# Kernel optimization log

Hardware: AMD Instinct MI355X
Metric: run time of the kernel (lower is better)

## Reference

```python
import jax, jax.numpy as jnp
import numpy as np
import math

DIM_IN = 2
DIM_HIDDEN = 64
DIM_OUT = 16
NUM_LAYERS = 5  # num_layers-1 = 4 hidden SirenLayers per subnet + 1 last layer
W0 = 30.0
W0_INITIAL = 30.0
S0 = 0.0
C = 6.0
N_POINTS = 262144


def wire(w0, s0, z):
    # sin(w0*z) * exp(-(s0*z)^2)
    return jnp.sin(w0 * z) * jnp.exp(-jnp.square(s0 * z))


def setup_inputs() -> dict:
    key = jax.random.key(0)
    ks = jax.random.split(key, 8)
    # NOTE: source passes is_first=False for every layer, so init bound is
    # sqrt(c/dim_in)/layer_w0 for ALL layers (including the first).
    std0 = math.sqrt(C / DIM_IN) / W0_INITIAL
    stdh = math.sqrt(C / DIM_HIDDEN) / W0
    stdl = math.sqrt(C / DIM_HIDDEN) / W0
    u = lambda k, shape, s: jax.random.uniform(k, shape, jnp.float32, -s, s)
    nmid = NUM_LAYERS - 2  # hidden->hidden layers per subnet (3)
    return {
        "x": jax.random.uniform(ks[0], (N_POINTS, DIM_IN), jnp.float32),
        "W0m": u(ks[1], (DIM_OUT, DIM_HIDDEN, DIM_IN), std0),
        "b0": u(ks[2], (DIM_OUT, DIM_HIDDEN), std0),
        "Wm": u(ks[3], (nmid, DIM_OUT, DIM_HIDDEN, DIM_HIDDEN), stdh),
        "bm": u(ks[4], (nmid, DIM_OUT, DIM_HIDDEN), stdh),
        "Wl": u(ks[5], (DIM_OUT, DIM_HIDDEN), stdl),
        "bl": u(ks[6], (DIM_OUT,), stdl),
    }


def reference(x, W0m, b0, Wm, bm, Wl, bl):
    # First layer of each subnet (uses w0_initial): [N,D] x [O,H,D] -> [N,O,H]
    h = wire(W0_INITIAL, S0, jnp.einsum("nd,ohd->noh", x, W0m) + b0)
    # Middle hidden layers (w0), scanned over the fixed layer stack.
    def body(h, wb):
        W, b = wb
        h = wire(W0, S0, jnp.einsum("noh,ogh->nog", h, W) + b)
        return h, None
    h, _ = jax.lax.scan(body, h, (Wm, bm))
    # Last layer per subnet: dim 1 output each, is_last -> +0.5, no activation.
    out = jnp.einsum("noh,oh->no", h, Wl) + bl + 0.5  # [N, dim_out]
    return out
```

## Files before the change

### kernel.cpp

```cpp
#include <hip/hip_runtime.h>

typedef short bf16x8 __attribute__((ext_vector_type(8)));
typedef float f32x16 __attribute__((ext_vector_type(16)));
typedef float f32x2  __attribute__((ext_vector_type(2)));

#define NBGROUPS 128
#define SCALE 4.7746482927568601f

union Frag { bf16x8 v; unsigned u[4]; uint4 q; };

__device__ __forceinline__ unsigned pk_bf16(float lo, float hi) {
    unsigned r;
    asm("v_cvt_pk_bf16_f32 %0, %1, %2" : "=v"(r) : "v"(lo), "v"(hi));
    return r;
}
__device__ __forceinline__ float lo_f(unsigned w) { return __uint_as_float(w << 16); }
__device__ __forceinline__ float hi_f(unsigned w) { return __uint_as_float(w & 0xffff0000u); }

__device__ __forceinline__ f32x2 sin2(f32x2 z) {
    f32x2 r  = { rintf(z.x), rintf(z.y) };
    f32x2 v  = z - r;
    f32x2 v2 = v * v;
    f32x2 p  = { 32.765379f, 32.765379f };
    p = __builtin_elementwise_fma(p, v2, (f32x2){-74.468884f, -74.468884f});
    p = __builtin_elementwise_fma(p, v2, (f32x2){ 81.365064f,  81.365064f});
    p = __builtin_elementwise_fma(p, v2, (f32x2){-41.331084f, -41.331084f});
    p = __builtin_elementwise_fma(p, v2, (f32x2){  6.2830526f,  6.2830526f});
    return p * v;
}

struct BiasRegs { f32x2 p[2][8]; };
__device__ __forceinline__ BiasRegs load_bias(const float4* ldsBias, int Lb, int hi) {
    BiasRegs br;
#pragma unroll
    for (int tg = 0; tg < 2; ++tg) {
        const float4* base = &ldsBias[((Lb*2+tg)*2 + hi)*4];
#pragma unroll
        for (int q = 0; q < 4; ++q) {
            float4 b = base[q];
            br.p[tg][2*q]   = (f32x2){b.x, b.y};
            br.p[tg][2*q+1] = (f32x2){b.z, b.w};
        }
    }
    return br;
}

__device__ __forceinline__ void transitionHL(const f32x16* acc, const BiasRegs& br,
                                             Frag* Bhi, Frag* Blo) {
#pragma unroll
    for (int tg = 0; tg < 2; ++tg)
#pragma unroll
        for (int j = 0; j < 8; ++j) {
            f32x2 z = (f32x2){ acc[tg][2*j], acc[tg][2*j+1] } + br.p[tg][j];
            f32x2 s = sin2(z);
            unsigned ph = pk_bf16(s.x, s.y);
            f32x2 hf = { lo_f(ph), hi_f(ph) };
            f32x2 d  = s - hf;
            Bhi[tg*2 + (j>>2)].u[j&3] = ph;
            Blo[tg*2 + (j>>2)].u[j&3] = pk_bf16(d.x, d.y);
        }
}
__device__ __forceinline__ void transitionH(const f32x16* acc, const BiasRegs& br, Frag* Bhi) {
#pragma unroll
    for (int tg = 0; tg < 2; ++tg)
#pragma unroll
        for (int j = 0; j < 8; ++j) {
            f32x2 z = (f32x2){ acc[tg][2*j], acc[tg][2*j+1] } + br.p[tg][j];
            f32x2 s = sin2(z);
            Bhi[tg*2 + (j>>2)].u[j&3] = pk_bf16(s.x, s.y);
        }
}

__device__ __forceinline__ void layerHL(f32x16* acc, const Frag* Bhi, const Frag* Blo,
                                        const uint4* ldsAhi, const uint4* ldsAlo,
                                        int L, int lane, const f32x16& zero16) {
    __builtin_amdgcn_s_setprio(1);
#pragma unroll
    for (int c = 0; c < 4; ++c) {
        Frag Ah0, Ah1, Al0, Al1;
        Ah0.q = ldsAhi[((L*2+0)*4+c)*64 + lane];
        Ah1.q = ldsAhi[((L*2+1)*4+c)*64 + lane];
        Al0.q = ldsAlo[((L*2+0)*4+c)*64 + lane];
        Al1.q = ldsAlo[((L*2+1)*4+c)*64 + lane];
        acc[0] = __builtin_amdgcn_mfma_f32_32x32x16_bf16(Ah0.v, Bhi[c].v, (c==0)?zero16:acc[0], 0, 0, 0);
        acc[1] = __builtin_amdgcn_mfma_f32_32x32x16_bf16(Ah1.v, Bhi[c].v, (c==0)?zero16:acc[1], 0, 0, 0);
        acc[0] = __builtin_amdgcn_mfma_f32_32x32x16_bf16(Ah0.v, Blo[c].v, acc[0], 0, 0, 0);
        acc[1] = __builtin_amdgcn_mfma_f32_32x32x16_bf16(Ah1.v, Blo[c].v, acc[1], 0, 0, 0);
        acc[0] = __builtin_amdgcn_mfma_f32_32x32x16_bf16(Al0.v, Bhi[c].v, acc[0], 0, 0, 0);
        acc[1] = __builtin_amdgcn_mfma_f32_32x32x16_bf16(Al1.v, Bhi[c].v, acc[1], 0, 0, 0);
    }
    __builtin_amdgcn_s_setprio(0);
}
__device__ __forceinline__ void layerH(f32x16* acc, const Frag* Bhi,
                                       const uint4* ldsAhi, int L, int lane,
                                       const f32x16& zero16) {
    __builtin_amdgcn_s_setprio(1);
#pragma unroll
    for (int c = 0; c < 4; ++c) {
        Frag Ah0, Ah1;
        Ah0.q = ldsAhi[((L*2+0)*4+c)*64 + lane];
        Ah1.q = ldsAhi[((L*2+1)*4+c)*64 + lane];
        acc[0] = __builtin_amdgcn_mfma_f32_32x32x16_bf16(Ah0.v, Bhi[c].v, (c==0)?zero16:acc[0], 0, 0, 0);
        acc[1] = __builtin_amdgcn_mfma_f32_32x32x16_bf16(Ah1.v, Bhi[c].v, (c==0)?zero16:acc[1], 0, 0, 0);
    }
    __builtin_amdgcn_s_setprio(0);
}

__global__ __launch_bounds__(256, 2)
void siren_kernel(const float* __restrict__ x, const float* __restrict__ W0m,
                  const float* __restrict__ b0, const float* __restrict__ Wm,
                  const float* __restrict__ bm, const float* __restrict__ Wl,
                  const float* __restrict__ bl, float* __restrict__ out)
{
    __shared__ uint4  ldsAhi[3*2*4*64];
    __shared__ uint4  ldsAlo[2*2*4*64];
    __shared__ float4 ldsBias[4*2*2*4];
    __shared__ float  ldsWl[2][32];

    const int tid  = threadIdx.x;
    const int pg   = blockIdx.x;
    const int o    = blockIdx.y;
    const int lane = tid & 63;
    const int wv   = tid >> 6;
    const int col  = lane & 31;
    const int hi   = lane >> 5;

    for (int idx = tid; idx < 3*2*4*64; idx += 256) {
        int l2  = idx & 63;
        int fi  = idx >> 6;
        int c   = fi & 3;
        int tg  = (fi >> 2) & 1;
        int L   = fi >> 3;
        int hi2 = l2 >> 5;
        int g   = tg*32 + (l2 & 31);
        int th  = c >> 1, s = c & 1;
        const float2* Wrow2 = (const float2*)(Wm + (((size_t)(L*16 + o)*64 + g)*64));
        uint4 whi, wlo;
        unsigned* uh = (unsigned*)&whi;
        unsigned* ul = (unsigned*)&wlo;
#pragma unroll
        for (int wi = 0; wi < 4; ++wi) {
            int h = th*32 + s*16 + 8*(wi>>1) + 2*(wi&1) + 4*hi2;
            float2 wp = Wrow2[h >> 1];
            float a = SCALE*wp.x, b = SCALE*wp.y;
            unsigned ph = pk_bf16(a, b);
            uh[wi] = ph;
            ul[wi] = pk_bf16(a - lo_f(ph), b - hi_f(ph));
        }
        ldsAhi[idx] = whi;
        if (idx < 2*2*4*64) ldsAlo[idx] = wlo;
    }
    if (tid < 64) {
        int q   = tid & 3;
        int hi2 = (tid >> 2) & 1;
        int tg  = (tid >> 3) & 1;
        int Lb  = tid >> 4;
        int h0  = tg*32 + 8*q + 4*hi2;
        const float* bsrc = (Lb < 3) ? (bm + (Lb*16 + o)*64) : (b0 + o*64);
        ldsBias[tid] = make_float4(SCALE*bsrc[h0], SCALE*bsrc[h0+1],
                                   SCALE*bsrc[h0+2], SCALE*bsrc[h0+3]);
    }
    if (tid >= 64 && tid < 128) {
        int t2  = tid - 64;
        int hi2 = t2 >> 5;
        int idx = t2 & 31;
        int tg  = idx >> 4;
        int r   = idx & 15;
        int s = r >> 3, j = r & 7;
        int h = tg*32 + 16*s + (j & 3) + 8*(j >> 2) + 4*hi2;
        ldsWl[hi2][idx] = Wl[o*64 + h];
    }

    Frag L1A[2];
#pragma unroll
    for (int tg = 0; tg < 2; ++tg) {
        int g = tg*32 + col;
        float2 wp = ((const float2*)W0m)[o*64 + g];
        float s0 = SCALE*wp.x, s1 = SCALE*wp.y;
        unsigned u0 = pk_bf16(s0, s0), u1 = pk_bf16(s1, s1);
        float l0 = s0 - lo_f(u0), l1 = s1 - lo_f(u1);
        L1A[tg].u[0] = hi ? 0u : u0;
        L1A[tg].u[1] = hi ? 0u : u1;
        L1A[tg].u[2] = hi ? 0u : pk_bf16(l0, l0);
        L1A[tg].u[3] = hi ? 0u : pk_bf16(l1, l1);
    }
    const float blv = bl[o] + 0.5f;

    f32x16 zero16;
#pragma unroll
    for (int i = 0; i < 16; ++i) zero16[i] = 0.f;

    __syncthreads();

    const int tbase = pg*64 + wv;
#pragma unroll 1
    for (int k = 0; k < 8; ++k) {
        const int ta  = tbase + 8*k;
        const int ppa = ta*32 + col;
        const int ppb = ppa + 128;

        float2 xa = ((const float2*)x)[ppa];
        float2 xb = ((const float2*)x)[ppb];
        Frag B1a, B1b;
        {
            unsigned ux = pk_bf16(xa.x, xa.y);
            float x0h = lo_f(ux), x1h = hi_f(ux);
            unsigned w0 = pk_bf16(x0h, xa.x - x0h);
            unsigned w1 = pk_bf16(x1h, xa.y - x1h);
            B1a.u[0] = hi ? 0u : w0;  B1a.u[1] = hi ? 0u : w1;
            B1a.u[2] = hi ? 0u : w0;  B1a.u[3] = hi ? 0u : w1;
            ux = pk_bf16(xb.x, xb.y);
            x0h = lo_f(ux); x1h = hi_f(ux);
            w0 = pk_bf16(x0h, xb.x - x0h);
            w1 = pk_bf16(x1h, xb.y - x1h);
            B1b.u[0] = hi ? 0u : w0;  B1b.u[1] = hi ? 0u : w1;
            B1b.u[2] = hi ? 0u : w0;  B1b.u[3] = hi ? 0u : w1;
        }

        BiasRegs br3 = load_bias(ldsBias, 3, hi);
        f32x16 accA[2], accB[2];

        __builtin_amdgcn_s_setprio(1);
        accA[0] = __builtin_amdgcn_mfma_f32_32x32x16_bf16(L1A[0].v, B1a.v, zero16, 0, 0, 0);
        accA[1] = __builtin_amdgcn_mfma_f32_32x32x16_bf16(L1A[1].v, B1a.v, zero16, 0, 0, 0);
        accB[0] = __builtin_amdgcn_mfma_f32_32x32x16_bf16(L1A[0].v, B1b.v, zero16, 0, 0, 0);
        accB[1] = __builtin_amdgcn_mfma_f32_32x32x16_bf16(L1A[1].v, B1b.v, zero16, 0, 0, 0);
        __builtin_amdgcn_s_setprio(0);

        Frag BhiA[4], BloA[4], BhiB[4], BloB[4];
        transitionHL(accA, br3, BhiA, BloA);
        layerHL(accA, BhiA, BloA, ldsAhi, ldsAlo, 0, lane, zero16);
        transitionHL(accB, br3, BhiB, BloB);
        layerHL(accB, BhiB, BloB, ldsAhi, ldsAlo, 0, lane, zero16);
        BiasRegs br0 = load_bias(ldsBias, 0, hi);
        transitionHL(accA, br0, BhiA, BloA);
        layerHL(accA, BhiA, BloA, ldsAhi, ldsAlo, 1, lane, zero16);
        transitionHL(accB, br0, BhiB, BloB);
        layerHL(accB, BhiB, BloB, ldsAhi, ldsAlo, 1, lane, zero16);
        BiasRegs br1 = load_bias(ldsBias, 1, hi);
        transitionH(accA, br1, BhiA);
        layerH(accA, BhiA, ldsAhi, 2, lane, zero16);
        transitionH(accB, br1, BhiB);
        layerH(accB, BhiB, ldsAhi, 2, lane, zero16);

        BiasRegs br2 = load_bias(ldsBias, 2, hi);
        const f32x2* wl2 = (const f32x2*)&ldsWl[hi][0];
        f32x2 sa = {0.f, 0.f}, sb = {0.f, 0.f};
#pragma unroll
        for (int tg = 0; tg < 2; ++tg)
#pragma unroll
            for (int j = 0; j < 8; ++j) {
                f32x2 w = wl2[tg*8 + j];
                f32x2 za = (f32x2){ accA[tg][2*j], accA[tg][2*j+1] } + br2.p[tg][j];
                f32x2 zb = (f32x2){ accB[tg][2*j], accB[tg][2*j+1] } + br2.p[tg][j];
                sa = __builtin_elementwise_fma(sin2(za), w, sa);
                sb = __builtin_elementwise_fma(sin2(zb), w, sb);
            }
        float suma = sa.x + sa.y;
        float sumb = sb.x + sb.y;
        suma += __shfl_xor(suma, 32);
        sumb += __shfl_xor(sumb, 32);
        if (lane < 32) {
            out[(size_t)ppa*16 + o] = suma + blv;
            out[(size_t)ppb*16 + o] = sumb + blv;
        }
    }
}

extern "C" void kernel_launch(void* const* d_in, const int* in_sizes, int n_in,
                              void* d_out, int out_size, void* d_ws, size_t ws_size,
                              hipStream_t stream) {
    (void)in_sizes; (void)n_in; (void)out_size; (void)d_ws; (void)ws_size;
    siren_kernel<<<dim3(NBGROUPS, 16), dim3(256), 0, stream>>>(
        (const float*)d_in[0], (const float*)d_in[1], (const float*)d_in[2],
        (const float*)d_in[3], (const float*)d_in[4], (const float*)d_in[5],
        (const float*)d_in[6], (float*)d_out);
}
```

Baseline: 369.2 us.

## Fold first-layer bias into MFMA, drop dual tiles, double block size

```diff
diff --git a/kernel.cpp b/kernel.cpp
--- a/kernel.cpp
+++ b/kernel.cpp
@@ -4,7 +4,7 @@
 typedef float f32x16 __attribute__((ext_vector_type(16)));
 typedef float f32x2  __attribute__((ext_vector_type(2)));
 
-#define NBGROUPS 128
+#define NBGROUPS 64
 #define SCALE 4.7746482927568601f
 
 union Frag { bf16x8 v; unsigned u[4]; uint4 q; };
@@ -45,6 +45,20 @@
     return br;
 }
 
+__device__ __forceinline__ void transition0HL(const f32x16* acc, Frag* Bhi, Frag* Blo) {
+#pragma unroll
+    for (int tg = 0; tg < 2; ++tg)
+#pragma unroll
+        for (int j = 0; j < 8; ++j) {
+            f32x2 z = { acc[tg][2*j], acc[tg][2*j+1] };
+            f32x2 s = sin2(z);
+            unsigned ph = pk_bf16(s.x, s.y);
+            f32x2 hf = { lo_f(ph), hi_f(ph) };
+            f32x2 d  = s - hf;
+            Bhi[tg*2 + (j>>2)].u[j&3] = ph;
+            Blo[tg*2 + (j>>2)].u[j&3] = pk_bf16(d.x, d.y);
+        }
+}
 __device__ __forceinline__ void transitionHL(const f32x16* acc, const BiasRegs& br,
                                              Frag* Bhi, Frag* Blo) {
 #pragma unroll
@@ -74,7 +88,6 @@
 __device__ __forceinline__ void layerHL(f32x16* acc, const Frag* Bhi, const Frag* Blo,
                                         const uint4* ldsAhi, const uint4* ldsAlo,
                                         int L, int lane, const f32x16& zero16) {
-    __builtin_amdgcn_s_setprio(1);
 #pragma unroll
     for (int c = 0; c < 4; ++c) {
         Frag Ah0, Ah1, Al0, Al1;
@@ -89,12 +102,10 @@
         acc[0] = __builtin_amdgcn_mfma_f32_32x32x16_bf16(Al0.v, Bhi[c].v, acc[0], 0, 0, 0);
         acc[1] = __builtin_amdgcn_mfma_f32_32x32x16_bf16(Al1.v, Bhi[c].v, acc[1], 0, 0, 0);
     }
-    __builtin_amdgcn_s_setprio(0);
 }
 __device__ __forceinline__ void layerH(f32x16* acc, const Frag* Bhi,
                                        const uint4* ldsAhi, int L, int lane,
                                        const f32x16& zero16) {
-    __builtin_amdgcn_s_setprio(1);
 #pragma unroll
     for (int c = 0; c < 4; ++c) {
         Frag Ah0, Ah1;
@@ -103,10 +114,9 @@
         acc[0] = __builtin_amdgcn_mfma_f32_32x32x16_bf16(Ah0.v, Bhi[c].v, (c==0)?zero16:acc[0], 0, 0, 0);
         acc[1] = __builtin_amdgcn_mfma_f32_32x32x16_bf16(Ah1.v, Bhi[c].v, (c==0)?zero16:acc[1], 0, 0, 0);
     }
-    __builtin_amdgcn_s_setprio(0);
-}
-
-__global__ __launch_bounds__(256, 2)
+}
+
+__global__ __launch_bounds__(512, 4)
 void siren_kernel(const float* __restrict__ x, const float* __restrict__ W0m,
                   const float* __restrict__ b0, const float* __restrict__ Wm,
                   const float* __restrict__ bm, const float* __restrict__ Wl,
@@ -114,7 +124,7 @@
 {
     __shared__ uint4  ldsAhi[3*2*4*64];
     __shared__ uint4  ldsAlo[2*2*4*64];
-    __shared__ float4 ldsBias[4*2*2*4];
+    __shared__ float4 ldsBias[3*2*2*4];
     __shared__ float  ldsWl[2][32];
 
     const int tid  = threadIdx.x;
@@ -125,7 +135,7 @@
     const int col  = lane & 31;
     const int hi   = lane >> 5;
 
-    for (int idx = tid; idx < 3*2*4*64; idx += 256) {
+    for (int idx = tid; idx < 3*2*4*64; idx += 512) {
         int l2  = idx & 63;
         int fi  = idx >> 6;
         int c   = fi & 3;
@@ -150,13 +160,13 @@
         ldsAhi[idx] = whi;
         if (idx < 2*2*4*64) ldsAlo[idx] = wlo;
     }
-    if (tid < 64) {
+    if (tid < 48) {
         int q   = tid & 3;
         int hi2 = (tid >> 2) & 1;
         int tg  = (tid >> 3) & 1;
         int Lb  = tid >> 4;
         int h0  = tg*32 + 8*q + 4*hi2;
-        const float* bsrc = (Lb < 3) ? (bm + (Lb*16 + o)*64) : (b0 + o*64);
+        const float* bsrc = bm + (Lb*16 + o)*64;
         ldsBias[tid] = make_float4(SCALE*bsrc[h0], SCALE*bsrc[h0+1],
                                    SCALE*bsrc[h0+2], SCALE*bsrc[h0+3]);
     }
@@ -177,12 +187,19 @@
         int g = tg*32 + col;
         float2 wp = ((const float2*)W0m)[o*64 + g];
         float s0 = SCALE*wp.x, s1 = SCALE*wp.y;
-        unsigned u0 = pk_bf16(s0, s0), u1 = pk_bf16(s1, s1);
-        float l0 = s0 - lo_f(u0), l1 = s1 - lo_f(u1);
+        float bias = SCALE*b0[o*64 + g];
+        unsigned u0 = pk_bf16(s0, s0);
+        float w0h = lo_f(u0);
+        float w0l = s0 - w0h;
+        unsigned t1 = pk_bf16(s1, s1);
+        float w1h = lo_f(t1);
+        float w1l = s1 - w1h;
+        unsigned ub = pk_bf16(bias, 0.f);
+        float bh = lo_f(ub), bl = bias - bh;
         L1A[tg].u[0] = hi ? 0u : u0;
-        L1A[tg].u[1] = hi ? 0u : u1;
-        L1A[tg].u[2] = hi ? 0u : pk_bf16(l0, l0);
-        L1A[tg].u[3] = hi ? 0u : pk_bf16(l1, l1);
+        L1A[tg].u[1] = hi ? 0u : pk_bf16(w0l, w1h);
+        L1A[tg].u[2] = hi ? 0u : pk_bf16(w1h, w1l);
+        L1A[tg].u[3] = hi ? 0u : pk_bf16(bh, bl);
     }
     const float blv = bl[o] + 0.5f;
 
@@ -192,78 +209,52 @@
 
     __syncthreads();
 
-    const int tbase = pg*64 + wv;
 #pragma unroll 1
-    for (int k = 0; k < 8; ++k) {
-        const int ta  = tbase + 8*k;
-        const int ppa = ta*32 + col;
-        const int ppb = ppa + 128;
-
-        float2 xa = ((const float2*)x)[ppa];
-        float2 xb = ((const float2*)x)[ppb];
-        Frag B1a, B1b;
+    for (int it = 0; it < 16; ++it) {
+        const int t  = pg*128 + it*8 + wv;
+        const int pp = t*32 + col;
+
+        float2 xv = ((const float2*)x)[pp];
+        Frag B1;
         {
-            unsigned ux = pk_bf16(xa.x, xa.y);
-            float x0h = lo_f(ux), x1h = hi_f(ux);
-            unsigned w0 = pk_bf16(x0h, xa.x - x0h);
-            unsigned w1 = pk_bf16(x1h, xa.y - x1h);
-            B1a.u[0] = hi ? 0u : w0;  B1a.u[1] = hi ? 0u : w1;
-            B1a.u[2] = hi ? 0u : w0;  B1a.u[3] = hi ? 0u : w1;
-            ux = pk_bf16(xb.x, xb.y);
-            x0h = lo_f(ux); x1h = hi_f(ux);
-            w0 = pk_bf16(x0h, xb.x - x0h);
-            w1 = pk_bf16(x1h, xb.y - x1h);
-            B1b.u[0] = hi ? 0u : w0;  B1b.u[1] = hi ? 0u : w1;
-            B1b.u[2] = hi ? 0u : w0;  B1b.u[3] = hi ? 0u : w1;
-        }
-
-        BiasRegs br3 = load_bias(ldsBias, 3, hi);
-        f32x16 accA[2], accB[2];
-
-        __builtin_amdgcn_s_setprio(1);
-        accA[0] = __builtin_amdgcn_mfma_f32_32x32x16_bf16(L1A[0].v, B1a.v, zero16, 0, 0, 0);
-        accA[1] = __builtin_amdgcn_mfma_f32_32x32x16_bf16(L1A[1].v, B1a.v, zero16, 0, 0, 0);
-        accB[0] = __builtin_amdgcn_mfma_f32_32x32x16_bf16(L1A[0].v, B1b.v, zero16, 0, 0, 0);
-        accB[1] = __builtin_amdgcn_mfma_f32_32x32x16_bf16(L1A[1].v, B1b.v, zero16, 0, 0, 0);
-        __builtin_amdgcn_s_setprio(0);
-
-        Frag BhiA[4], BloA[4], BhiB[4], BloB[4];
-        transitionHL(accA, br3, BhiA, BloA);
-        layerHL(accA, BhiA, BloA, ldsAhi, ldsAlo, 0, lane, zero16);
-        transitionHL(accB, br3, BhiB, BloB);
-        layerHL(accB, BhiB, BloB, ldsAhi, ldsAlo, 0, lane, zero16);
+            unsigned u0 = pk_bf16(xv.x, xv.x);
+            float x0h = lo_f(u0), x0l = xv.x - x0h;
+            unsigned u1 = pk_bf16(xv.y, xv.y);
+            float x1h = lo_f(u1), x1l = xv.y - x1h;
+            B1.u[0] = pk_bf16(x0h, x0l);
+            B1.u[1] = pk_bf16(x0h, x1h);
+            B1.u[2] = pk_bf16(x1l, x1h);
+            B1.u[3] = 0x3f803f80u;
+        }
+
+        f32x16 acc[2];
+        acc[0] = __builtin_amdgcn_mfma_f32_32x32x16_bf16(L1A[0].v, B1.v, zero16, 0, 0, 0);
+        acc[1] = __builtin_amdgcn_mfma_f32_32x32x16_bf16(L1A[1].v, B1.v, zero16, 0, 0, 0);
+
+        Frag Bhi[4], Blo[4];
+        transition0HL(acc, Bhi, Blo);
+        layerHL(acc, Bhi, Blo, ldsAhi, ldsAlo, 0, lane, zero16);
         BiasRegs br0 = load_bias(ldsBias, 0, hi);
-        transitionHL(accA, br0, BhiA, BloA);
-        layerHL(accA, BhiA, BloA, ldsAhi, ldsAlo, 1, lane, zero16);
-        transitionHL(accB, br0, BhiB, BloB);
-        layerHL(accB, BhiB, BloB, ldsAhi, ldsAlo, 1, lane, zero16);
+        transitionHL(acc, br0, Bhi, Blo);
+        layerHL(acc, Bhi, Blo, ldsAhi, ldsAlo, 1, lane, zero16);
         BiasRegs br1 = load_bias(ldsBias, 1, hi);
-        transitionH(accA, br1, BhiA);
-        layerH(accA, BhiA, ldsAhi, 2, lane, zero16);
-        transitionH(accB, br1, BhiB);
-        layerH(accB, BhiB, ldsAhi, 2, lane, zero16);
+        transitionH(acc, br1, Bhi);
+        layerH(acc, Bhi, ldsAhi, 2, lane, zero16);
 
         BiasRegs br2 = load_bias(ldsBias, 2, hi);
         const f32x2* wl2 = (const f32x2*)&ldsWl[hi][0];
-        f32x2 sa = {0.f, 0.f}, sb = {0.f, 0.f};
+        f32x2 sa = {0.f, 0.f};
 #pragma unroll
         for (int tg = 0; tg < 2; ++tg)
 #pragma unroll
             for (int j = 0; j < 8; ++j) {
                 f32x2 w = wl2[tg*8 + j];
-                f32x2 za = (f32x2){ accA[tg][2*j], accA[tg][2*j+1] } + br2.p[tg][j];
-                f32x2 zb = (f32x2){ accB[tg][2*j], accB[tg][2*j+1] } + br2.p[tg][j];
+                f32x2 za = (f32x2){ acc[tg][2*j], acc[tg][2*j+1] } + br2.p[tg][j];
                 sa = __builtin_elementwise_fma(sin2(za), w, sa);
-                sb = __builtin_elementwise_fma(sin2(zb), w, sb);
             }
         float suma = sa.x + sa.y;
-        float sumb = sb.x + sb.y;
         suma += __shfl_xor(suma, 32);
-        sumb += __shfl_xor(sumb, 32);
-        if (lane < 32) {
-            out[(size_t)ppa*16 + o] = suma + blv;
-            out[(size_t)ppb*16 + o] = sumb + blv;
-        }
+        if (lane < 32) out[(size_t)pp*16 + o] = suma + blv;
     }
 }
 
@@ -271,7 +262,7 @@
                               void* d_out, int out_size, void* d_ws, size_t ws_size,
                               hipStream_t stream) {
     (void)in_sizes; (void)n_in; (void)out_size; (void)d_ws; (void)ws_size;
-    siren_kernel<<<dim3(NBGROUPS, 16), dim3(256), 0, stream>>>(
+    siren_kernel<<<dim3(NBGROUPS, 16), dim3(512), 0, stream>>>(
         (const float*)d_in[0], (const float*)d_in[1], (const float*)d_in[2],
         (const float*)d_in[3], (const float*)d_in[4], (const float*)d_in[5],
         (const float*)d_in[6], (float*)d_out);
```

Result: faster. 357.8 us (-3.1%).
